# Kernel tuning notes

Measured on AMD Instinct MI355X. Metric: run time of the kernel, lower is better.

## Reference

```python
import jax, jax.numpy as jnp
import numpy as np

# Sparse MinkUNet-style backbone sizes
N0, N1, N2, N3 = 100000, 50000, 25000, 12500  # voxels per level (batch-concatenated)
K, KD = 27, 8        # 3x3x3 kernel offsets, stride-2 child offsets
B, S = 8, 1024       # batch, seed_num
C0, C1, C2, C3 = 32, 64, 128, 256
COUT = 512


def _w(k, shape, fan_in):
    return jax.random.normal(k, shape, dtype=jnp.float32) / np.sqrt(fan_in)


def setup_inputs() -> dict:
    key = jax.random.key(0)
    ks = jax.random.split(key, 32)
    inp = {}
    inp["feats"] = jax.random.normal(ks[0], (N0, 3), dtype=jnp.float32)
    # neighbor maps (kernel-offset gather indices, as built by a voxel hash map)
    inp["nbr0"] = jax.random.randint(ks[1], (N0, K), 0, N0, dtype=jnp.int32)
    inp["nbr1"] = jax.random.randint(ks[2], (N1, K), 0, N1, dtype=jnp.int32)
    inp["nbr2"] = jax.random.randint(ks[3], (N2, K), 0, N2, dtype=jnp.int32)
    inp["nbr3"] = jax.random.randint(ks[4], (N3, K), 0, N3, dtype=jnp.int32)
    # stride-2 downsample maps (coarse voxel -> fine children)
    inp["down1"] = jax.random.randint(ks[5], (N1, KD), 0, N0, dtype=jnp.int32)
    inp["down2"] = jax.random.randint(ks[6], (N2, KD), 0, N1, dtype=jnp.int32)
    inp["down3"] = jax.random.randint(ks[7], (N3, KD), 0, N2, dtype=jnp.int32)
    # nearest-parent upsample maps (fine voxel -> coarse parent)
    inp["up2"] = jax.random.randint(ks[8], (N2,), 0, N3, dtype=jnp.int32)
    inp["up1"] = jax.random.randint(ks[9], (N1,), 0, N2, dtype=jnp.int32)
    inp["up0"] = jax.random.randint(ks[10], (N0,), 0, N1, dtype=jnp.int32)
    # nearest-voxel devoxelize index for each FPS seed point
    inp["seed_idx"] = jax.random.randint(ks[11], (B, S), 0, N0, dtype=jnp.int32)
    # conv kernels [K, Cin, Cout] and 1x1 (linear) decoder weights
    inp["W_stem"] = _w(ks[12], (K, 3, C0), K * 3)
    inp["W_b0"] = _w(ks[13], (K, C0, C0), K * C0)
    inp["W_d1"] = _w(ks[14], (KD, C0, C1), KD * C0)
    inp["W_b1"] = _w(ks[15], (K, C1, C1), K * C1)
    inp["W_d2"] = _w(ks[16], (KD, C1, C2), KD * C1)
    inp["W_b2"] = _w(ks[17], (K, C2, C2), K * C2)
    inp["W_d3"] = _w(ks[18], (KD, C2, C3), KD * C2)
    inp["W_b3"] = _w(ks[19], (K, C3, C3), K * C3)
    inp["W_u2"] = _w(ks[20], (C3 + C2, 256), C3 + C2)
    inp["W_u1"] = _w(ks[21], (256 + C1, 128), 256 + C1)
    inp["W_u0"] = _w(ks[22], (128 + C0, 96), 128 + C0)
    inp["W_out"] = _w(ks[23], (96, COUT), 96)
    return inp


def sp_conv(f, nbr, W):
    # gather neighbor features then contract over (kernel offset, in-channel)
    g = f[nbr]                                # [N, K, Cin]
    return jnp.einsum('nkc,kco->no', g, W)    # [N, Cout]


def reference(feats, nbr0, nbr1, nbr2, nbr3, down1, down2, down3,
              up2, up1, up0, seed_idx,
              W_stem, W_b0, W_d1, W_b1, W_d2, W_b2, W_d3, W_b3,
              W_u2, W_u1, W_u0, W_out):
    relu = jax.nn.relu
    # encoder
    x0 = relu(sp_conv(feats, nbr0, W_stem))          # [N0, 32]
    x0 = x0 + relu(sp_conv(x0, nbr0, W_b0))
    x1 = relu(sp_conv(x0, down1, W_d1))              # [N1, 64]
    x1 = x1 + relu(sp_conv(x1, nbr1, W_b1))
    x2 = relu(sp_conv(x1, down2, W_d2))              # [N2, 128]
    x2 = x2 + relu(sp_conv(x2, nbr2, W_b2))
    x3 = relu(sp_conv(x2, down3, W_d3))              # [N3, 256]
    x3 = x3 + relu(sp_conv(x3, nbr3, W_b3))
    # decoder: nearest-parent upsample + skip concat + 1x1 conv
    u2 = relu(jnp.concatenate([x3[up2], x2], axis=-1) @ W_u2)   # [N2, 256]
    u1 = relu(jnp.concatenate([u2[up1], x1], axis=-1) @ W_u1)   # [N1, 128]
    u0 = relu(jnp.concatenate([u1[up0], x0], axis=-1) @ W_u0)   # [N0, 96]
    out_vox = u0 @ W_out                                        # [N0, 512]
    seed_feats = out_vox[seed_idx]                              # [B, S, 512]
    return jnp.transpose(seed_feats, (0, 2, 1))                 # [B, 512, S]
```

## Files before the change

kernel.cpp:

```cpp
#include <hip/hip_runtime.h>

typedef unsigned short u16;
typedef unsigned int u32;
typedef __bf16 bf16x8 __attribute__((ext_vector_type(8)));
typedef float f32x4 __attribute__((ext_vector_type(4)));
typedef u16 u16x4 __attribute__((ext_vector_type(4)));

#define NV0 100000
#define NV1 50000
#define NV2 25000
#define NV3 12500

enum : long {
  OFF_WB0  = 0,
  OFF_WD1  = 27648,
  OFF_WB1  = 44032,
  OFF_WD2  = 154624,
  OFF_WB2  = 220160,
  OFF_WD3  = 662528,
  OFF_WB3  = 924672,
  OFF_WU2  = 2694144,
  OFF_WU1  = 2792448,
  OFF_WU0  = 2833408,
  OFF_WOUT = 2848768,
  OFF_TA   = 2897920,
  OFF_X0   = OFF_TA  + 3200000,
  OFF_X1   = OFF_X0  + 3200000,
  OFF_X2   = OFF_X1  + 3200000,
  OFF_X3   = OFF_X2  + 3200000,
  OFF_U2   = OFF_X3  + 3200000,
  OFF_U1   = OFF_U2  + 6400000,
  OFF_U0S  = OFF_U1  + 6400000,
  OFF_END  = OFF_U0S + 786432,
};

__device__ __forceinline__ float b2f(u16 u) {
  union { u32 i; float f; } x; x.i = ((u32)u) << 16; return x.f;
}
__device__ __forceinline__ u16 f2b(float f) {
  union { float f; u32 i; } x; x.f = f;
  u32 r = (x.i + 0x7FFFu + ((x.i >> 16) & 1u)) >> 16;
  return (u16)r;
}
__device__ __forceinline__ void gload16(const u16* g, const u16* l) {
  __builtin_amdgcn_global_load_lds(
      (const __attribute__((address_space(1))) void*)g,
      (__attribute__((address_space(3))) void*)(u16*)l, 16, 0, 0);
}
__device__ __forceinline__ void store_out(u16* p, float v)  { *p = f2b(v); }
__device__ __forceinline__ void store_out(float* p, float v) { *p = v; }
constexpr int ilog2c(int x) { return x <= 1 ? 0 : 1 + ilog2c(x / 2); }

struct PD { const float* src; u16* dst; int KK, CIN, COUT; };
struct PrepArgs { PD d[11]; };

__global__ __launch_bounds__(256) void prep_k(PrepArgs pa) {
  const PD d = pa.d[blockIdx.y];
  const int cc = d.CIN * d.COUT;
  const int total = d.KK * cc;
  for (int e = blockIdx.x * 256 + threadIdx.x; e < total; e += gridDim.x * 256) {
    int k = e / cc;
    int r = e - k * cc;
    int c = r / d.COUT;
    int o = r - c * d.COUT;
    d.dst[(k * d.COUT + o) * d.CIN + c] = f2b(d.src[e]);
  }
}

__global__ __launch_bounds__(256) void stem_k(const float* __restrict__ feats,
                                              const int* __restrict__ nbr0,
                                              const float* __restrict__ wstem,
                                              u16* __restrict__ out) {
  __shared__ float Wl[27 * 3 * 32];
  const int tid = threadIdx.x;
  for (int i = tid; i < 2592; i += 256) Wl[i] = wstem[i];
  __syncthreads();
  const int n = blockIdx.x * 8 + (tid >> 5);
  const int o = tid & 31;
  if (n >= NV0) return;
  float acc = 0.f;
  const int* nb = nbr0 + n * 27;
  #pragma unroll
  for (int k = 0; k < 27; k++) {
    const int iv = nb[k];
    const float* f = feats + iv * 3;
    acc = fmaf(f[0], Wl[(k * 3 + 0) * 32 + o], acc);
    acc = fmaf(f[1], Wl[(k * 3 + 1) * 32 + o], acc);
    acc = fmaf(f[2], Wl[(k * 3 + 2) * 32 + o], acc);
  }
  out[n * 32 + o] = f2b(fmaxf(acc, 0.f));
}

template <int BM, int BN, int WM, int WN, int COUTF, int KCT, int BK, int MODE,
          int CIN, int KK, int KSP, int CA, bool RES, bool DORELU, bool PARTIAL,
          int MINW, typename OT>
__global__ __launch_bounds__(256, MINW) void gemm_k(
    const u16* __restrict__ src0, const u16* __restrict__ src1,
    const int* __restrict__ idx0, const int* __restrict__ idx1,
    const u16* __restrict__ wt, const u16* __restrict__ base,
    OT* __restrict__ out, int N) {
  constexpr int NWM = BM / WM, NWN = BN / WN;
  static_assert(NWM * NWN == 4, "4 waves");
  constexpr int MI = WM / 16, NI = WN / 16;
  constexpr int CB = KCT - CA;
  constexpr int SLOTS = BK / 8;
  constexpr int SM = SLOTS - 1;
  constexpr int LSL = ilog2c(SLOTS);
  constexpr int RPC = 64 / SLOTS;
  constexpr int LRPC = ilog2c(RPC);
  constexpr int ACH = (BM * BK) / 512;
  constexpr int BCH = (BN * BK) / 512;
  constexpr int LOGC = ilog2c(CIN);
  constexpr int LBM = ilog2c(BM);
  constexpr int NIDX = (MODE == 0) ? BM * KSP : (MODE == 1 ? BM : (MODE == 2 ? 2 * BM : 1));
  static_assert(KCT % BK == 0, "K mult of BK");
  static_assert(MODE != 1 || (CA % BK == 0), "concat boundary aligned");

  __shared__ u16 As[2][BM * BK];
  __shared__ u16 Bs[2][BN * BK];
  __shared__ int Is[NIDX];
  const int tid = threadIdx.x;
  const int w = tid >> 6, lane = tid & 63;
  const int quad = lane >> 4, l16 = lane & 15;
  const int wm = w % NWM, wn = w / NWM;
  const int row0 = blockIdx.x * BM;
  const int col0 = blockIdx.y * BN;
  const int Nm1 = N - 1;
  const int k0 = (MODE == 0) ? (int)blockIdx.z * KSP : 0;
  const int k1 = (MODE == 0) ? ((k0 + KSP > KK) ? KK : k0 + KSP) : 0;
  const int kcb = (MODE == 0) ? k0 * CIN : 0;
  const int kce = (MODE == 0) ? k1 * CIN : KCT;
  if constexpr (PARTIAL) out += (long)blockIdx.z * N * COUTF;
  const int srow = lane >> LSL;
  const int g    = (lane & SM) ^ (srow & SM);
  const int cl   = g * 8;

  if constexpr (MODE == 0) {
    const int kcnt = k1 - k0;
    for (int e = tid; e < kcnt * BM; e += 256) {
      const int kl = e >> LBM, r = e & (BM - 1);
      int n = row0 + r; n = (n > Nm1) ? Nm1 : n;
      Is[e] = idx0[(long)n * KK + k0 + kl];
    }
  } else if constexpr (MODE == 1) {
    for (int e = tid; e < BM; e += 256) {
      int n = row0 + e; n = (n > Nm1) ? Nm1 : n;
      Is[e] = idx0[n];
    }
  } else if constexpr (MODE == 2) {
    for (int e = tid; e < BM; e += 256) {
      int n = row0 + e; n = (n > Nm1) ? Nm1 : n;
      const int s = idx0[n];
      Is[e] = idx1[s];
      Is[BM + e] = s;
    }
  }
  if constexpr (MODE != 3) __syncthreads();

  f32x4 acc[MI][NI];
  #pragma unroll
  for (int i = 0; i < MI; i++)
    #pragma unroll
    for (int j = 0; j < NI; j++) acc[i][j] = {0.f, 0.f, 0.f, 0.f};

  auto stage = [&](int buf, int kc0) {
    for (int c = w; c < ACH + BCH; c += 4) {
      const int cab = kc0 + cl;
      if (c < ACH) {
        const int r = (c << LRPC) + srow;
        const u16* gp;
        if constexpr (MODE == 0) {
          const int k = cab >> LOGC;
          gp = src0 + (long)Is[((k - k0) << LBM) | r] * CIN + (cab & (CIN - 1));
        } else if constexpr (MODE == 1) {
          if (kc0 < CA) gp = src0 + (long)Is[r] * CA + cab;
          else {
            int n = row0 + r; n = (n > Nm1) ? Nm1 : n;
            gp = src1 + (long)n * CB + (cab - CA);
          }
        } else if constexpr (MODE == 2) {
          if (kc0 < CA) gp = src0 + (long)Is[r] * CA + cab;
          else          gp = src1 + (long)Is[BM + r] * CB + (cab - CA);
        } else {
          int n = row0 + r; n = (n > Nm1) ? Nm1 : n;
          gp = src0 + (long)n * KCT + cab;
        }
        gload16(gp, &As[buf][c * 512]);
      } else {
        const int cb = c - ACH;
        const int o = col0 + (cb << LRPC) + srow;
        const u16* gp;
        if constexpr (MODE == 0) {
          const int k = cab >> LOGC;
          gp = wt + ((long)(k * COUTF + o)) * CIN + (cab & (CIN - 1));
        } else {
          gp = wt + (long)o * KCT + cab;
        }
        gload16(gp, &Bs[buf][cb * 512]);
      }
    }
  };

  const int nit = (kce - kcb) / BK;
  stage(0, kcb);
  #pragma unroll 1
  for (int it = 0; it < nit; it++) {
    __syncthreads();
    if (it + 1 < nit) stage((it + 1) & 1, kcb + (it + 1) * BK);
    const int buf = it & 1;
    #pragma unroll
    for (int kk = 0; kk < BK / 32; kk++) {
      bf16x8 af[MI], bfr[NI];
      #pragma unroll
      for (int i = 0; i < MI; i++) {
        const int row = wm * WM + i * 16 + l16;
        const int slot = row * SLOTS + (((kk << 2) + quad) ^ (row & SM));
        af[i] = *(const bf16x8*)&As[buf][slot * 8];
      }
      #pragma unroll
      for (int j = 0; j < NI; j++) {
        const int row = wn * WN + j * 16 + l16;
        const int slot = row * SLOTS + (((kk << 2) + quad) ^ (row & SM));
        bfr[j] = *(const bf16x8*)&Bs[buf][slot * 8];
      }
      #pragma unroll
      for (int i = 0; i < MI; i++)
        #pragma unroll
        for (int j = 0; j < NI; j++)
          acc[i][j] = __builtin_amdgcn_mfma_f32_16x16x32_bf16(af[i], bfr[j], acc[i][j], 0, 0, 0);
    }
  }

  #pragma unroll
  for (int i = 0; i < MI; i++) {
    #pragma unroll
    for (int j = 0; j < NI; j++) {
      const int col = col0 + wn * WN + j * 16 + l16;
      #pragma unroll
      for (int r = 0; r < 4; r++) {
        const int n = row0 + wm * WM + i * 16 + quad * 4 + r;
        if (n < N) {
          float v = acc[i][j][r];
          if constexpr (RES)         v = b2f(base[(long)n * COUTF + col]) + fmaxf(v, 0.f);
          else if constexpr (DORELU) v = fmaxf(v, 0.f);
          store_out(&out[(long)n * COUTF + col], v);
        }
      }
    }
  }
}

__global__ __launch_bounds__(256) void comb_k(const float* __restrict__ P,
                                              const u16* __restrict__ base,
                                              u16* __restrict__ out, int total) {
  const int i = (blockIdx.x * 256 + threadIdx.x) * 4;
  if (i >= total) return;
  const f32x4 a = *(const f32x4*)&P[i];
  const f32x4 b = *(const f32x4*)&P[total + i];
  u16x4 o;
  #pragma unroll
  for (int j = 0; j < 4; j++)
    o[j] = f2b(b2f(base[i + j]) + fmaxf(a[j] + b[j], 0.f));
  *(u16x4*)&out[i] = o;
}

__global__ __launch_bounds__(256) void tout_k(const float* __restrict__ tmp,
                                              float* __restrict__ outp) {
  __shared__ float tl[64][65];
  const int tid = threadIdx.x;
  const int r0 = blockIdx.x * 64, o0 = blockIdx.y * 64;
  {
    const int rl = tid >> 2, oc = (tid & 3) * 16;
    const float* src = &tmp[(r0 + rl) * 512 + o0 + oc];
    #pragma unroll
    for (int j = 0; j < 16; j++) tl[rl][oc + j] = src[j];
  }
  __syncthreads();
  {
    const int ol = tid >> 2, sc = (tid & 3) * 16;
    const int b = r0 >> 10, s0 = r0 & 1023;
    float* dst = &outp[((long)b * 512 + (o0 + ol)) * 1024 + s0 + sc];
    #pragma unroll
    for (int j = 0; j < 16; j++) dst[j] = tl[sc + j][ol];
  }
}

extern "C" void kernel_launch(void* const* d_in, const int* in_sizes, int n_in,
                              void* d_out, int out_size, void* d_ws, size_t ws_size,
                              hipStream_t stream) {
  const float* feats = (const float*)d_in[0];
  const int* nbr0  = (const int*)d_in[1];
  const int* nbr1  = (const int*)d_in[2];
  const int* nbr2  = (const int*)d_in[3];
  const int* nbr3  = (const int*)d_in[4];
  const int* down1 = (const int*)d_in[5];
  const int* down2 = (const int*)d_in[6];
  const int* down3 = (const int*)d_in[7];
  const int* up2   = (const int*)d_in[8];
  const int* up1   = (const int*)d_in[9];
  const int* up0   = (const int*)d_in[10];
  const int* seed  = (const int*)d_in[11];
  u16* ws = (u16*)d_ws;

  PrepArgs pa;
  pa.d[0]  = {(const float*)d_in[13], ws + OFF_WB0,  27, 32, 32};
  pa.d[1]  = {(const float*)d_in[14], ws + OFF_WD1,  8,  32, 64};
  pa.d[2]  = {(const float*)d_in[15], ws + OFF_WB1,  27, 64, 64};
  pa.d[3]  = {(const float*)d_in[16], ws + OFF_WD2,  8,  64, 128};
  pa.d[4]  = {(const float*)d_in[17], ws + OFF_WB2,  27, 128, 128};
  pa.d[5]  = {(const float*)d_in[18], ws + OFF_WD3,  8,  128, 256};
  pa.d[6]  = {(const float*)d_in[19], ws + OFF_WB3,  27, 256, 256};
  pa.d[7]  = {(const float*)d_in[20], ws + OFF_WU2,  1,  384, 256};
  pa.d[8]  = {(const float*)d_in[21], ws + OFF_WU1,  1,  320, 128};
  pa.d[9]  = {(const float*)d_in[22], ws + OFF_WU0,  1,  160, 96};
  pa.d[10] = {(const float*)d_in[23], ws + OFF_WOUT, 1,  96,  512};
  prep_k<<<dim3(128, 11), 256, 0, stream>>>(pa);

  u16* ta  = ws + OFF_TA;
  u16* x0  = ws + OFF_X0;
  u16* x1  = ws + OFF_X1;
  u16* x2  = ws + OFF_X2;
  u16* x3  = ws + OFF_X3;
  u16* u2b = ws + OFF_U2;
  u16* u1b = ws + OFF_U1;
  u16* u0s = ws + OFF_U0S;
  float* P   = (float*)(ws + OFF_U2);
  float* tmp = (float*)(ws + OFF_TA);

  stem_k<<<12500, 256, 0, stream>>>(feats, nbr0, (const float*)d_in[12], ta);

  gemm_k<128, 32, 32, 32, 32, 864, 32, 0, 32, 27, 27, 0, true, true, false, 4, u16>
      <<<dim3(782, 1, 1), 256, 0, stream>>>(ta, nullptr, nbr0, nullptr, ws + OFF_WB0, ta, x0, NV0);
  gemm_k<128, 64, 64, 32, 64, 256, 64, 0, 32, 8, 8, 0, false, true, false, 4, u16>
      <<<dim3(391, 1, 1), 256, 0, stream>>>(x0, nullptr, down1, nullptr, ws + OFF_WD1, nullptr, ta, NV1);
  gemm_k<128, 64, 64, 32, 64, 1728, 32, 0, 64, 27, 27, 0, true, true, false, 4, u16>
      <<<dim3(391, 1, 1), 256, 0, stream>>>(ta, nullptr, nbr1, nullptr, ws + OFF_WB1, ta, x1, NV1);
  gemm_k<64, 128, 32, 64, 128, 512, 64, 0, 64, 8, 8, 0, false, true, false, 4, u16>
      <<<dim3(391, 1, 1), 256, 0, stream>>>(x1, nullptr, down2, nullptr, ws + OFF_WD2, nullptr, ta, NV2);
  gemm_k<128, 128, 64, 64, 128, 3456, 32, 0, 128, 27, 14, 0, false, false, true, 2, float>
      <<<dim3(196, 1, 2), 256, 0, stream>>>(ta, nullptr, nbr2, nullptr, ws + OFF_WB2, nullptr, P, NV2);
  comb_k<<<dim3(3125), 256, 0, stream>>>(P, ta, x2, NV2 * 128);
  gemm_k<64, 128, 32, 64, 256, 1024, 64, 0, 128, 8, 8, 0, false, true, false, 4, u16>
      <<<dim3(196, 2, 1), 256, 0, stream>>>(x2, nullptr, down3, nullptr, ws + OFF_WD3, nullptr, ta, NV3);
  gemm_k<128, 128, 64, 64, 256, 6912, 32, 0, 256, 27, 14, 0, false, false, true, 2, float>
      <<<dim3(98, 2, 2), 256, 0, stream>>>(ta, nullptr, nbr3, nullptr, ws + OFF_WB3, nullptr, P, NV3);
  comb_k<<<dim3(3125), 256, 0, stream>>>(P, ta, x3, NV3 * 256);
  gemm_k<64, 128, 32, 64, 256, 384, 64, 1, 32, 1, 1, 256, false, true, false, 4, u16>
      <<<dim3(391, 2, 1), 256, 0, stream>>>(x3, x2, up2, nullptr, ws + OFF_WU2, nullptr, u2b, NV2);
  gemm_k<64, 128, 32, 64, 128, 320, 64, 1, 32, 1, 1, 256, false, true, false, 4, u16>
      <<<dim3(782, 1, 1), 256, 0, stream>>>(u2b, x1, up1, nullptr, ws + OFF_WU1, nullptr, u1b, NV1);
  gemm_k<64, 96, 32, 48, 96, 160, 32, 2, 32, 1, 1, 128, false, true, false, 4, u16>
      <<<dim3(128, 1, 1), 256, 0, stream>>>(u1b, x0, seed, up0, ws + OFF_WU0, nullptr, u0s, 8192);
  gemm_k<64, 128, 32, 64, 512, 96, 32, 3, 32, 1, 1, 0, false, false, false, 4, float>
      <<<dim3(128, 4, 1), 256, 0, stream>>>(u0s, nullptr, nullptr, nullptr, ws + OFF_WOUT, nullptr, tmp, 8192);
  tout_k<<<dim3(128, 8), 256, 0, stream>>>(tmp, (float*)d_out);
}
```

Before: 540.5 us.

## Rework LDS swizzle layout for BK=32 tiles and retune GEMM tile configs

Replaces the XOR swizzle of the shared-memory A/B tiles with a per-BK layout. The BK=32 case now uses a row-pair-interleaved layout meant to avoid LDS bank conflicts on the fragment reads, and address computation is centralised in a helper. Several launches also change: occupancy hints drop from 4 to 2 or 3, the nbr1 conv moves to BK=64, and the decoder 1x1 GEMMs switch to 128x128 tiles with BK=32 and fewer blocks. The staging and read layouts must stay consistent with each other, and the larger tiles reduce the number of blocks available for parallelism.

```diff
diff --git a/kernel.cpp b/kernel.cpp
--- a/kernel.cpp
+++ b/kernel.cpp
@@ -101,11 +101,10 @@
     OT* __restrict__ out, int N) {
   constexpr int NWM = BM / WM, NWN = BN / WN;
   static_assert(NWM * NWN == 4, "4 waves");
+  static_assert(BK == 32 || BK == 64, "BK 32/64");
   constexpr int MI = WM / 16, NI = WN / 16;
   constexpr int CB = KCT - CA;
   constexpr int SLOTS = BK / 8;
-  constexpr int SM = SLOTS - 1;
-  constexpr int LSL = ilog2c(SLOTS);
   constexpr int RPC = 64 / SLOTS;
   constexpr int LRPC = ilog2c(RPC);
   constexpr int ACH = (BM * BK) / 512;
@@ -131,9 +130,14 @@
   const int kcb = (MODE == 0) ? k0 * CIN : 0;
   const int kce = (MODE == 0) ? k1 * CIN : KCT;
   if constexpr (PARTIAL) out += (long)blockIdx.z * N * COUTF;
-  const int srow = lane >> LSL;
-  const int g    = (lane & SM) ^ (srow & SM);
-  const int cl   = g * 8;
+  int srow, cl;
+  if constexpr (SLOTS == 4) {
+    srow = ((lane >> 3) << 1) | (lane & 1);
+    cl   = ((lane >> 1) & 3) * 8;
+  } else {
+    srow = lane >> 3;
+    cl   = ((lane & 7) ^ (srow & 7)) * 8;
+  }
 
   if constexpr (MODE == 0) {
     const int kcnt = k1 - k0;
@@ -201,6 +205,13 @@
     }
   };
 
+  auto faddr = [&](int row, int kk) -> int {
+    if constexpr (SLOTS == 4)
+      return ((row >> 4) << 9) + (((row >> 1) & 7) << 6) + ((row & 1) << 3) + (quad << 4);
+    else
+      return (row << 6) + (((((kk << 2) + quad)) ^ (row & 7)) << 3);
+  };
+
   const int nit = (kce - kcb) / BK;
   stage(0, kcb);
   #pragma unroll 1
@@ -212,17 +223,11 @@
     for (int kk = 0; kk < BK / 32; kk++) {
       bf16x8 af[MI], bfr[NI];
       #pragma unroll
-      for (int i = 0; i < MI; i++) {
-        const int row = wm * WM + i * 16 + l16;
-        const int slot = row * SLOTS + (((kk << 2) + quad) ^ (row & SM));
-        af[i] = *(const bf16x8*)&As[buf][slot * 8];
-      }
+      for (int i = 0; i < MI; i++)
+        af[i] = *(const bf16x8*)&As[buf][faddr(wm * WM + i * 16 + l16, kk)];
       #pragma unroll
-      for (int j = 0; j < NI; j++) {
-        const int row = wn * WN + j * 16 + l16;
-        const int slot = row * SLOTS + (((kk << 2) + quad) ^ (row & SM));
-        bfr[j] = *(const bf16x8*)&Bs[buf][slot * 8];
-      }
+      for (int j = 0; j < NI; j++)
+        bfr[j] = *(const bf16x8*)&Bs[buf][faddr(wn * WN + j * 16 + l16, kk)];
       #pragma unroll
       for (int i = 0; i < MI; i++)
         #pragma unroll
@@ -331,24 +336,24 @@
 
   gemm_k<128, 32, 32, 32, 32, 864, 32, 0, 32, 27, 27, 0, true, true, false, 4, u16>
       <<<dim3(782, 1, 1), 256, 0, stream>>>(ta, nullptr, nbr0, nullptr, ws + OFF_WB0, ta, x0, NV0);
-  gemm_k<128, 64, 64, 32, 64, 256, 64, 0, 32, 8, 8, 0, false, true, false, 4, u16>
+  gemm_k<128, 64, 64, 32, 64, 256, 64, 0, 32, 8, 8, 0, false, true, false, 2, u16>
       <<<dim3(391, 1, 1), 256, 0, stream>>>(x0, nullptr, down1, nullptr, ws + OFF_WD1, nullptr, ta, NV1);
-  gemm_k<128, 64, 64, 32, 64, 1728, 32, 0, 64, 27, 27, 0, true, true, false, 4, u16>
+  gemm_k<128, 64, 64, 32, 64, 1728, 64, 0, 64, 27, 27, 0, true, true, false, 2, u16>
       <<<dim3(391, 1, 1), 256, 0, stream>>>(ta, nullptr, nbr1, nullptr, ws + OFF_WB1, ta, x1, NV1);
-  gemm_k<64, 128, 32, 64, 128, 512, 64, 0, 64, 8, 8, 0, false, true, false, 4, u16>
+  gemm_k<64, 128, 32, 64, 128, 512, 64, 0, 64, 8, 8, 0, false, true, false, 2, u16>
       <<<dim3(391, 1, 1), 256, 0, stream>>>(x1, nullptr, down2, nullptr, ws + OFF_WD2, nullptr, ta, NV2);
   gemm_k<128, 128, 64, 64, 128, 3456, 32, 0, 128, 27, 14, 0, false, false, true, 2, float>
       <<<dim3(196, 1, 2), 256, 0, stream>>>(ta, nullptr, nbr2, nullptr, ws + OFF_WB2, nullptr, P, NV2);
   comb_k<<<dim3(3125), 256, 0, stream>>>(P, ta, x2, NV2 * 128);
-  gemm_k<64, 128, 32, 64, 256, 1024, 64, 0, 128, 8, 8, 0, false, true, false, 4, u16>
+  gemm_k<64, 128, 32, 64, 256, 1024, 64, 0, 128, 8, 8, 0, false, true, false, 2, u16>
       <<<dim3(196, 2, 1), 256, 0, stream>>>(x2, nullptr, down3, nullptr, ws + OFF_WD3, nullptr, ta, NV3);
   gemm_k<128, 128, 64, 64, 256, 6912, 32, 0, 256, 27, 14, 0, false, false, true, 2, float>
       <<<dim3(98, 2, 2), 256, 0, stream>>>(ta, nullptr, nbr3, nullptr, ws + OFF_WB3, nullptr, P, NV3);
   comb_k<<<dim3(3125), 256, 0, stream>>>(P, ta, x3, NV3 * 256);
-  gemm_k<64, 128, 32, 64, 256, 384, 64, 1, 32, 1, 1, 256, false, true, false, 4, u16>
-      <<<dim3(391, 2, 1), 256, 0, stream>>>(x3, x2, up2, nullptr, ws + OFF_WU2, nullptr, u2b, NV2);
-  gemm_k<64, 128, 32, 64, 128, 320, 64, 1, 32, 1, 1, 256, false, true, false, 4, u16>
-      <<<dim3(782, 1, 1), 256, 0, stream>>>(u2b, x1, up1, nullptr, ws + OFF_WU1, nullptr, u1b, NV1);
+  gemm_k<128, 128, 64, 64, 256, 384, 32, 1, 32, 1, 1, 256, false, true, false, 3, u16>
+      <<<dim3(196, 2, 1), 256, 0, stream>>>(x3, x2, up2, nullptr, ws + OFF_WU2, nullptr, u2b, NV2);
+  gemm_k<128, 128, 64, 64, 128, 320, 32, 1, 32, 1, 1, 256, false, true, false, 3, u16>
+      <<<dim3(391, 1, 1), 256, 0, stream>>>(u2b, x1, up1, nullptr, ws + OFF_WU1, nullptr, u1b, NV1);
   gemm_k<64, 96, 32, 48, 96, 160, 32, 2, 32, 1, 1, 128, false, true, false, 4, u16>
       <<<dim3(128, 1, 1), 256, 0, stream>>>(u1b, x0, seed, up0, ws + OFF_WU0, nullptr, u0s, 8192);
   gemm_k<64, 128, 32, 64, 512, 96, 32, 3, 32, 1, 1, 0, false, false, false, 4, float>
```

Result: no change. 536.6 us (-0.7%).
